# Kernel optimization log

Measured on AMD Instinct MI355X. Metric: run time of the kernel, lower is better.

The kernel has to match this reference:

```python
import math
import jax, jax.numpy as jnp
import numpy as np

# ---- MnnCoreModule constants (mnn_config defaults) ----
L = 0.05          # conductance
SL = math.sqrt(L)
VT = 20.0         # vol_th
VR = 0.0          # vol_rest
TREF = 5.0        # t_ref
CUT = 10.0        # cut_off
SQRT_PI_HALF = 0.8862269254527580


def _gl01(n):
    x, w = np.polynomial.legendre.leggauss(n)
    return (jnp.asarray((x + 1.0) / 2.0, jnp.float32),
            jnp.asarray(w / 2.0, jnp.float32))

A48, WA48 = _gl01(48)   # 1D quadrature nodes for G(x), E(x)
A32, WA32 = _gl01(32)   # outer nodes for H(x)
B32, WB32 = _gl01(32)   # inner nodes for H_pos
Q32, WQ32 = _gl01(32)   # nodes for semi-infinite inner integral (H_neg)
R32 = -jnp.log1p(-Q32)  # r = -log(1-q) maps (0,1) -> (0,inf)


def g_fn(x):
    """func_dawson: g(x) = sqrt(pi)/2 * exp(x^2) * (1 + erf(x)).
    Uses the asymptotic erfcx expansion for x << 0 (numerically stable)."""
    d = jnp.where(x >= -3.0, x, 0.0)
    direct = SQRT_PI_HALF * jnp.exp(d * d) * (1.0 + jax.scipy.special.erf(d))
    z = jnp.where(x < -3.0, -x, 3.0)
    z2 = z * z
    asym = (0.5 / z) * (1.0 - 0.5 / z2 + 0.75 / (z2 * z2) - 1.875 / (z2 * z2 * z2))
    return jnp.where(x >= -3.0, direct, asym)


def G_fn(x):
    """dawson1: G(x) = int_0^x g(t) dt (48-pt Gauss-Legendre, scaled)."""
    t = x[..., None] * A48
    return x * jnp.sum(WA48 * g_fn(t), axis=-1)


def E_fn(x):
    """int_0^x exp(t^2) dt for x >= 0."""
    t = x[..., None] * A48
    return x * jnp.sum(WA48 * jnp.exp(t * t), axis=-1)

# C0 = int_{-inf}^0 exp(-s^2) g(s)^2 ds (constant, high-accuracy quadrature)
_Q64, _WQ64 = _gl01(64)
_R64 = -jnp.log1p(-_Q64)
C0 = jnp.sum(_WQ64 * jnp.exp(-_R64 * _R64) * g_fn(-_R64) ** 2 / (1.0 - _Q64))


def _h_neg(t):
    """h(t) = exp(t^2) int_{-inf}^t exp(-s^2) g(s)^2 ds for t <= 0,
    via s = t - r, r = -log(1-q):  h(t) = int exp(2tr - r^2) g(t-r)^2 dr."""
    tt = t[..., None]
    integ = jnp.exp(2.0 * tt * R32 - R32 * R32) * g_fn(tt - R32) ** 2 / (1.0 - Q32)
    return jnp.sum(WQ32 * integ, axis=-1)


def H_neg(x):
    """double Dawson integral H(x) = int_0^x h(t) dt for x <= 0."""
    def step(aw):
        ai, wi = aw
        return wi * _h_neg(x * ai)
    terms = jax.lax.map(jax.checkpoint(step), (A32, WA32))  # [Ka, ...]
    return x * jnp.sum(terms, axis=0)


def H_pos(x):
    """H(x) for x >= 0: H = C0*E(x) + iint_{0<=s<=t<=x} e^{t^2-s^2} g(s)^2."""
    def step(aw):
        ai, wi = aw
        t = x * ai
        s = t[..., None] * B32
        inner = jnp.sum(WB32 * jnp.exp(-s * s) * g_fn(s) ** 2, axis=-1)
        return wi * ai * jnp.exp(t * t) * inner
    terms = jax.lax.map(jax.checkpoint(step), (A32, WA32))
    return C0 * E_fn(x) + x * x * jnp.sum(terms, axis=0)


def H_fn(x):
    return jnp.where(x >= 0.0, H_pos(jnp.maximum(x, 0.0)), H_neg(jnp.minimum(x, 0.0)))


def setup_inputs() -> dict:
    key = jax.random.key(0)
    k1, k2 = jax.random.split(key)
    u = 0.5 + jax.random.uniform(k1, (128, 1024), dtype=jnp.float32)  # [0.5, 1.5)
    raw = jax.random.uniform(k2, (128, 1024), dtype=jnp.float32) * 2.9
    s = jnp.where(raw < 0.4, 0.0, raw)
    return {"u": u, "s": s}


def reference(u, s):
    # region masks (mirrors _region0_idx)
    reg1 = (s > 0.0) & ((VT * L - u) < CUT * SL * s)
    reg0 = ~(s > 0.0)
    reg2 = reg0 & (u > VT * L)

    s_safe = jnp.where(reg1, s, 1.0)
    ub = jnp.where(reg1, (VT * L - u) / (SL * s_safe), 1.0)
    lb = jnp.where(reg1, (VR * L - u) / (SL * s_safe), 0.0)  # always <= 0

    # mean firing rate u_a
    dG = G_fn(ub) - G_fn(lb)
    u_a1 = 1.0 / ((2.0 / L) * dG + TREF)
    u2 = jnp.where(reg2, u, 2.0)
    logt = TREF - (1.0 / L) * jnp.log(1.0 - 1.0 / u2)
    u_a = jnp.where(reg1, u_a1, jnp.where(reg2, 1.0 / logt, 0.0))

    # std s_a via Fano factor
    dH = H_fn(ub) - H_neg(jnp.minimum(lb, 0.0))
    fano = jnp.where(reg1, (8.0 / (L * L)) * dH * u_a * u_a,
                     jnp.where(reg0, (u < 1.0).astype(u.dtype), 0.0))
    val = fano * u_a
    s_a = jnp.where(val > 0.0, jnp.sqrt(jnp.where(val > 0.0, val, 1.0)), 0.0)

    # linear response chi
    dg = g_fn(ub) - g_fn(lb)
    sa_safe = jnp.where(reg1 & (s_a > 0.0), s_a, 1.0)
    chi1 = u_a * u_a / sa_safe * dg * (2.0 / L ** 1.5)
    chi2 = math.sqrt(2.0 / L) / jnp.sqrt(logt) / jnp.sqrt(2.0 * u2 - 1.0)
    chi = jnp.where(reg1, chi1, jnp.where(reg2, chi2, 0.0))
    return (u_a, s_a, chi)
```

## Files before the change

kernel.cpp:

```cpp
#include <hip/hip_runtime.h>
#include <math.h>

#define SLf   0.22360679774997896f

#define NTAB   2048
#define XMIN   -17.0
#define XMAX   6.0
#define XMINf  -17.0f
#define DXf    (23.0f / 2047.0f)
#define INVDXf (2047.0f / 23.0f)

__device__ double dd_A48[48], dd_W48[48];
__device__ double dd_A32[32], dd_W32[32];
__device__ double dd_R32[32], dd_WQE32[32];
__device__ float f_A48[48], f_W48[48];
__device__ float f_A32[32], f_W32[32];
__device__ float f_R32[32], f_WQE32[32];
__device__ float f_C0;

__device__ float  htabf[NTAB];
__device__ float  innertabf[NTAB];
__device__ float4 tab4[NTAB];

__device__ double g_dbl(double x) {
    if (x >= -3.0) return 0.8862269254527580 * exp(x * x) * (1.0 + erf(x));
    double z = -x, iz2 = 1.0 / (z * z);
    return (0.5 / z) * (1.0 + iz2 * (-0.5 + iz2 * (0.75 - 1.875 * iz2)));
}

__device__ __forceinline__ float g_f32(float x) {
    if (x >= -3.0f) {
        return 0.88622692545275801f * __expf(x * x) * erfcf(-x);
    }
    float z = -x, iz = 1.0f / z, iz2 = iz * iz;
    return 0.5f * iz * (1.0f + iz2 * (-0.5f + iz2 * (0.75f - 1.875f * iz2)));
}

template <int N>
__device__ void gl_node_t(int i, const double* __restrict__ inv, double* x01, double* w01) {
    double z = cos(3.14159265358979323846 * ((double)i + 0.75) / ((double)N + 0.5));
    double pl = z, pm = 1.0, pp = 1.0;
    for (int it = 0; it < 6; ++it) {
        pm = 1.0; pl = z;
        #pragma unroll
        for (int k = 2; k <= N; ++k) {
            double pk = ((2.0 * k - 1.0) * z * pl - (k - 1.0) * pm) * inv[k];
            pm = pl; pl = pk;
        }
        pp = (double)N * (z * pl - pm) / (z * z - 1.0);
        z -= pl / pp;
    }
    pm = 1.0; pl = z;
    #pragma unroll
    for (int k = 2; k <= N; ++k) {
        double pk = ((2.0 * k - 1.0) * z * pl - (k - 1.0) * pm) * inv[k];
        pm = pl; pl = pk;
    }
    pp = (double)N * (z * pl - pm) / (z * z - 1.0);
    *x01 = 0.5 * (z + 1.0);
    *w01 = 1.0 / ((1.0 - z * z) * pp * pp);
}

__global__ void init_nodes() {
    __shared__ double s_inv[65];
    int i = threadIdx.x;
    if (i >= 2 && i <= 64) s_inv[i] = 1.0 / (double)i;
    __syncthreads();

    if (i < 48) {
        double x, w; gl_node_t<48>(i, s_inv, &x, &w);
        dd_A48[i] = x; dd_W48[i] = w;
        f_A48[i] = (float)x; f_W48[i] = (float)w;
    } else if (i >= 64 && i < 96) {
        int j = i - 64;
        double x, w; gl_node_t<32>(j, s_inv, &x, &w);
        dd_A32[j] = x; dd_W32[j] = w;
        f_A32[j] = (float)x; f_W32[j] = (float)w;
        f_R32[j] = (float)(-log1p(-x));
        f_WQE32[j] = (float)(w / (1.0 - x));
    } else if (i >= 128 && i < 192) {
        int j = i - 128;
        double x, w; gl_node_t<64>(j, s_inv, &x, &w);
        double r = -log1p(-x);
        double gv = g_dbl(-r);
        double term = w * exp(-r * r) * gv * gv / (1.0 - x);
        for (int off = 32; off > 0; off >>= 1)
            term += __shfl_down(term, off);
        if (j == 0) f_C0 = (float)term;
    }
}

__global__ __launch_bounds__(256) void init_tabs() {
    int gid = blockIdx.x * blockDim.x + threadIdx.x;
    int k = gid >> 2, p = gid & 3;
    if (k >= NTAB) return;
    float x = XMINf + DXf * (float)k;

    float aG = 0.0f;
    for (int q = 12 * p; q < 12 * p + 12; ++q)
        aG = fmaf(f_W48[q], g_f32(x * f_A48[q]), aG);

    float ah = 0.0f;
    for (int j = 8 * p; j < 8 * p + 8; ++j) {
        float r = f_R32[j];
        float gg = g_f32(x - r);
        ah = fmaf(f_WQE32[j], __expf((2.0f * x - r) * r) * gg * gg, ah);
    }

    float ai = 0.0f;
    for (int j = 8 * p; j < 8 * p + 8; ++j) {
        float s = x * f_A32[j];
        float gs = g_f32(s);
        ai = fmaf(f_W32[j], __expf(-s * s) * gs * gs, ai);
    }

    aG += __shfl_xor(aG, 1, 4); aG += __shfl_xor(aG, 2, 4);
    ah += __shfl_xor(ah, 1, 4); ah += __shfl_xor(ah, 2, 4);
    ai += __shfl_xor(ai, 1, 4); ai += __shfl_xor(ai, 2, 4);

    if (p == 0) {
        htabf[k] = ah;
        innertabf[k] = ai;
        float4 t; t.x = g_f32(x); t.y = x * aG; t.z = 0.0f; t.w = 0.0f;
        tab4[k] = t;
    }
}

__device__ __forceinline__ float interp1(const float* __restrict__ tab, float x) {
    float u = (x - XMINf) * INVDXf;
    u = fminf(fmaxf(u, 1.0f), (float)(NTAB - 3));
    int k = (int)u;
    if (k > NTAB - 3) k = NTAB - 3;
    float f = u - (float)k;
    float p0 = tab[k - 1], p1 = tab[k], p2 = tab[k + 1], p3 = tab[k + 2];
    return p1 + 0.5f * f * (p2 - p0 + f * (2.0f * p0 - 5.0f * p1 + 4.0f * p2 - p3
                 + f * (3.0f * (p1 - p2) + p3 - p0)));
}

__global__ __launch_bounds__(256) void init_H() {
    int gid = blockIdx.x * blockDim.x + threadIdx.x;
    int k = gid >> 2, p = gid & 3;
    if (k >= NTAB) return;
    float x = XMINf + DXf * (float)k;

    float H;
    if (x < 0.0f) {
        float acc = 0.0f;
        for (int i = 8 * p; i < 8 * p + 8; ++i)
            acc = fmaf(f_W32[i], interp1(htabf, x * f_A32[i]), acc);
        acc += __shfl_xor(acc, 1, 4); acc += __shfl_xor(acc, 2, 4);
        H = x * acc;
    } else {
        float aE = 0.0f;
        for (int q = 12 * p; q < 12 * p + 12; ++q) {
            float t = x * f_A48[q];
            aE = fmaf(f_W48[q], __expf(t * t), aE);
        }
        float aS = 0.0f;
        for (int i = 8 * p; i < 8 * p + 8; ++i) {
            float t = x * f_A32[i];
            aS = fmaf(f_W32[i] * f_A32[i], __expf(t * t) * interp1(innertabf, t), aS);
        }
        aE += __shfl_xor(aE, 1, 4); aE += __shfl_xor(aE, 2, 4);
        aS += __shfl_xor(aS, 1, 4); aS += __shfl_xor(aS, 2, 4);
        H = f_C0 * (x * aE) + x * x * aS;
    }
    if (p == 0) tab4[k].z = H;
}

__device__ __forceinline__ void cr_weights(float x, int* kk, float* w) {
    float u = (x - XMINf) * INVDXf;
    u = fminf(fmaxf(u, 1.0f), (float)(NTAB - 3));
    int k = (int)u;
    if (k > NTAB - 3) k = NTAB - 3;
    float f = u - (float)k;
    float f2 = f * f, f3 = f2 * f;
    w[0] = 0.5f * (-f + 2.0f * f2 - f3);
    w[1] = 1.0f + 0.5f * (-5.0f * f2 + 3.0f * f3);
    w[2] = 0.5f * (f + 4.0f * f2 - 3.0f * f3);
    w[3] = 0.5f * (f3 - f2);
    *kk = k;
}

__global__ __launch_bounds__(256) void mnn_main(const float* __restrict__ U,
        const float* __restrict__ S, float* __restrict__ out, int n) {
    int idx = blockIdx.x * blockDim.x + threadIdx.x;
    if (idx >= n) return;
    float u = U[idx], s = S[idx];
    float ua = 0.0f, sa = 0.0f, chi = 0.0f;

    bool sgt0 = (s > 0.0f);
    bool reg1 = sgt0 && ((1.0f - u) < 10.0f * SLf * s);

    if (reg1) {
        float inv = 1.0f / (SLf * s);
        float ub = (1.0f - u) * inv;
        float lb = -u * inv;

        int ku, kl; float wu[4], wl[4];
        cr_weights(ub, &ku, wu);
        cr_weights(lb, &kl, wl);
        float4 a0 = tab4[ku - 1], a1 = tab4[ku], a2 = tab4[ku + 1], a3 = tab4[ku + 2];
        float4 b0 = tab4[kl - 1], b1 = tab4[kl], b2 = tab4[kl + 1], b3 = tab4[kl + 2];

        float g_ub = wu[0]*a0.x + wu[1]*a1.x + wu[2]*a2.x + wu[3]*a3.x;
        float G_ub = wu[0]*a0.y + wu[1]*a1.y + wu[2]*a2.y + wu[3]*a3.y;
        float H_ub = wu[0]*a0.z + wu[1]*a1.z + wu[2]*a2.z + wu[3]*a3.z;
        float g_lb = wl[0]*b0.x + wl[1]*b1.x + wl[2]*b2.x + wl[3]*b3.x;
        float G_lb = wl[0]*b0.y + wl[1]*b1.y + wl[2]*b2.y + wl[3]*b3.y;
        float H_lb = wl[0]*b0.z + wl[1]*b1.z + wl[2]*b2.z + wl[3]*b3.z;

        float dG = G_ub - G_lb;
        float ua1 = 1.0f / (40.0f * dG + 5.0f);
        float dH = H_ub - H_lb;

        float fano = 3200.0f * dH * ua1 * ua1;
        float val = fano * ua1;
        float s_a = (val > 0.0f) ? sqrtf(val) : 0.0f;

        float dg = g_ub - g_lb;
        float sa_safe = (s_a > 0.0f) ? s_a : 1.0f;
        chi = ua1 * ua1 * dg * 178.88543819998318f / sa_safe;
        ua = ua1; sa = s_a;
    } else if (!sgt0 && u > 1.0f) {
        float logt = 5.0f - 20.0f * logf(1.0f - 1.0f / u);
        ua = 1.0f / logt;
        chi = 6.324555320336759f / (sqrtf(logt) * sqrtf(2.0f * u - 1.0f));
    }

    out[idx] = ua;
    out[n + idx] = sa;
    out[2 * n + idx] = chi;
}

extern "C" void kernel_launch(void* const* d_in, const int* in_sizes, int n_in,
                              void* d_out, int out_size, void* d_ws, size_t ws_size,
                              hipStream_t stream) {
    const float* u = (const float*)d_in[0];
    const float* s = (const float*)d_in[1];
    float* out = (float*)d_out;
    int n = in_sizes[0];

    init_nodes<<<dim3(1), dim3(256), 0, stream>>>();
    init_tabs<<<dim3((NTAB * 4 + 255) / 256), dim3(256), 0, stream>>>();
    init_H<<<dim3((NTAB * 4 + 255) / 256), dim3(256), 0, stream>>>();
    mnn_main<<<dim3((n + 255) / 256), dim3(256), 0, stream>>>(u, s, out, n);
}
```

Baseline: 30.51 us.

## Fuse three table-building kernels into one with per-block node generation

Replaces the init_nodes, init_tabs and init_H kernels with one build_tables kernel. Every block recomputes the Gauss-Legendre nodes into shared memory, and each 32-lane group builds one table entry. H is now computed by direct nested quadrature (32x32 g evaluations per entry) instead of interpolating from intermediate h/inner tables. This removes two kernel launches and their serialization, but adds redundant node computation in every block and much more arithmetic per table entry. Newton iterations for the nodes also drop from 6 to 4.

After: 29.13 us. 4.5% less time.

```diff
diff --git a/kernel.cpp b/kernel.cpp
--- a/kernel.cpp
+++ b/kernel.cpp
@@ -4,22 +4,10 @@
 #define SLf   0.22360679774997896f
 
 #define NTAB   2048
-#define XMIN   -17.0
-#define XMAX   6.0
 #define XMINf  -17.0f
 #define DXf    (23.0f / 2047.0f)
 #define INVDXf (2047.0f / 23.0f)
 
-__device__ double dd_A48[48], dd_W48[48];
-__device__ double dd_A32[32], dd_W32[32];
-__device__ double dd_R32[32], dd_WQE32[32];
-__device__ float f_A48[48], f_W48[48];
-__device__ float f_A32[32], f_W32[32];
-__device__ float f_R32[32], f_WQE32[32];
-__device__ float f_C0;
-
-__device__ float  htabf[NTAB];
-__device__ float  innertabf[NTAB];
 __device__ float4 tab4[NTAB];
 
 __device__ double g_dbl(double x) {
@@ -39,8 +27,8 @@
 template <int N>
 __device__ void gl_node_t(int i, const double* __restrict__ inv, double* x01, double* w01) {
     double z = cos(3.14159265358979323846 * ((double)i + 0.75) / ((double)N + 0.5));
-    double pl = z, pm = 1.0, pp = 1.0;
-    for (int it = 0; it < 6; ++it) {
+    double pl, pm, pp;
+    for (int it = 0; it < 4; ++it) {
         pm = 1.0; pl = z;
         #pragma unroll
         for (int k = 2; k <= N; ++k) {
@@ -61,111 +49,82 @@
     *w01 = 1.0 / ((1.0 - z * z) * pp * pp);
 }
 
-__global__ void init_nodes() {
+__global__ __launch_bounds__(256) void build_tables() {
     __shared__ double s_inv[65];
-    int i = threadIdx.x;
-    if (i >= 2 && i <= 64) s_inv[i] = 1.0 / (double)i;
+    __shared__ float sA48[48], sW48[48];
+    __shared__ float sA32[32], sW32[32], sR32[32], sWQ[32];
+    __shared__ float sC0;
+    int tid = threadIdx.x;
+    if (tid >= 2 && tid <= 64) s_inv[tid] = 1.0 / (double)tid;
     __syncthreads();
 
-    if (i < 48) {
-        double x, w; gl_node_t<48>(i, s_inv, &x, &w);
-        dd_A48[i] = x; dd_W48[i] = w;
-        f_A48[i] = (float)x; f_W48[i] = (float)w;
-    } else if (i >= 64 && i < 96) {
-        int j = i - 64;
+    if (tid < 48) {
+        double x, w; gl_node_t<48>(tid, s_inv, &x, &w);
+        sA48[tid] = (float)x; sW48[tid] = (float)w;
+    } else if (tid >= 64 && tid < 96) {
+        int j = tid - 64;
         double x, w; gl_node_t<32>(j, s_inv, &x, &w);
-        dd_A32[j] = x; dd_W32[j] = w;
-        f_A32[j] = (float)x; f_W32[j] = (float)w;
-        f_R32[j] = (float)(-log1p(-x));
-        f_WQE32[j] = (float)(w / (1.0 - x));
-    } else if (i >= 128 && i < 192) {
-        int j = i - 128;
+        sA32[j] = (float)x; sW32[j] = (float)w;
+        sR32[j] = (float)(-log1p(-x));
+        sWQ[j]  = (float)(w / (1.0 - x));
+    } else if (tid >= 128 && tid < 192) {
+        int j = tid - 128;
         double x, w; gl_node_t<64>(j, s_inv, &x, &w);
         double r = -log1p(-x);
         double gv = g_dbl(-r);
         double term = w * exp(-r * r) * gv * gv / (1.0 - x);
         for (int off = 32; off > 0; off >>= 1)
             term += __shfl_down(term, off);
-        if (j == 0) f_C0 = (float)term;
-    }
-}
-
-__global__ __launch_bounds__(256) void init_tabs() {
-    int gid = blockIdx.x * blockDim.x + threadIdx.x;
-    int k = gid >> 2, p = gid & 3;
-    if (k >= NTAB) return;
+        if (j == 0) sC0 = (float)term;
+    }
+    __syncthreads();
+
+    int k = blockIdx.x * 8 + (tid >> 5);
+    int i = tid & 31;
     float x = XMINf + DXf * (float)k;
 
-    float aG = 0.0f;
-    for (int q = 12 * p; q < 12 * p + 12; ++q)
-        aG = fmaf(f_W48[q], g_f32(x * f_A48[q]), aG);
-
-    float ah = 0.0f;
-    for (int j = 8 * p; j < 8 * p + 8; ++j) {
-        float r = f_R32[j];
-        float gg = g_f32(x - r);
-        ah = fmaf(f_WQE32[j], __expf((2.0f * x - r) * r) * gg * gg, ah);
-    }
-
-    float ai = 0.0f;
-    for (int j = 8 * p; j < 8 * p + 8; ++j) {
-        float s = x * f_A32[j];
-        float gs = g_f32(s);
-        ai = fmaf(f_W32[j], __expf(-s * s) * gs * gs, ai);
-    }
-
-    aG += __shfl_xor(aG, 1, 4); aG += __shfl_xor(aG, 2, 4);
-    ah += __shfl_xor(ah, 1, 4); ah += __shfl_xor(ah, 2, 4);
-    ai += __shfl_xor(ai, 1, 4); ai += __shfl_xor(ai, 2, 4);
-
-    if (p == 0) {
-        htabf[k] = ah;
-        innertabf[k] = ai;
-        float4 t; t.x = g_f32(x); t.y = x * aG; t.z = 0.0f; t.w = 0.0f;
-        tab4[k] = t;
-    }
-}
-
-__device__ __forceinline__ float interp1(const float* __restrict__ tab, float x) {
-    float u = (x - XMINf) * INVDXf;
-    u = fminf(fmaxf(u, 1.0f), (float)(NTAB - 3));
-    int k = (int)u;
-    if (k > NTAB - 3) k = NTAB - 3;
-    float f = u - (float)k;
-    float p0 = tab[k - 1], p1 = tab[k], p2 = tab[k + 1], p3 = tab[k + 2];
-    return p1 + 0.5f * f * (p2 - p0 + f * (2.0f * p0 - 5.0f * p1 + 4.0f * p2 - p3
-                 + f * (3.0f * (p1 - p2) + p3 - p0)));
-}
-
-__global__ __launch_bounds__(256) void init_H() {
-    int gid = blockIdx.x * blockDim.x + threadIdx.x;
-    int k = gid >> 2, p = gid & 3;
-    if (k >= NTAB) return;
-    float x = XMINf + DXf * (float)k;
-
-    float H;
+    float aG = sW48[i] * g_f32(x * sA48[i]);
+    if (i < 16) aG = fmaf(sW48[i + 32], g_f32(x * sA48[i + 32]), aG);
+
+    float Hp, aE = 0.0f;
+    float t = x * sA32[i];
     if (x < 0.0f) {
-        float acc = 0.0f;
-        for (int i = 8 * p; i < 8 * p + 8; ++i)
-            acc = fmaf(f_W32[i], interp1(htabf, x * f_A32[i]), acc);
-        acc += __shfl_xor(acc, 1, 4); acc += __shfl_xor(acc, 2, 4);
-        H = x * acc;
+        float h = 0.0f;
+        for (int j = 0; j < 32; ++j) {
+            float r = sR32[j];
+            float gg = g_f32(t - r);
+            h = fmaf(sWQ[j], __expf((2.0f * t - r) * r) * gg * gg, h);
+        }
+        Hp = sW32[i] * h;
     } else {
-        float aE = 0.0f;
-        for (int q = 12 * p; q < 12 * p + 12; ++q) {
-            float t = x * f_A48[q];
-            aE = fmaf(f_W48[q], __expf(t * t), aE);
-        }
-        float aS = 0.0f;
-        for (int i = 8 * p; i < 8 * p + 8; ++i) {
-            float t = x * f_A32[i];
-            aS = fmaf(f_W32[i] * f_A32[i], __expf(t * t) * interp1(innertabf, t), aS);
-        }
-        aE += __shfl_xor(aE, 1, 4); aE += __shfl_xor(aE, 2, 4);
-        aS += __shfl_xor(aS, 1, 4); aS += __shfl_xor(aS, 2, 4);
-        H = f_C0 * (x * aE) + x * x * aS;
-    }
-    if (p == 0) tab4[k].z = H;
+        float inner = 0.0f;
+        for (int j = 0; j < 32; ++j) {
+            float s = t * sA32[j];
+            float gs = g_f32(s);
+            inner = fmaf(sW32[j], __expf(-s * s) * gs * gs, inner);
+        }
+        Hp = sW32[i] * sA32[i] * __expf(t * t) * inner;
+        float t0 = x * sA48[i];
+        aE = sW48[i] * __expf(t0 * t0);
+        if (i < 16) {
+            float t1 = x * sA48[i + 32];
+            aE = fmaf(sW48[i + 32], __expf(t1 * t1), aE);
+        }
+    }
+
+    #pragma unroll
+    for (int off = 16; off > 0; off >>= 1) {
+        aG += __shfl_xor(aG, off, 32);
+        Hp += __shfl_xor(Hp, off, 32);
+        aE += __shfl_xor(aE, off, 32);
+    }
+
+    if (i == 0) {
+        float Hv = (x < 0.0f) ? x * Hp
+                              : sC0 * (x * aE) + x * x * Hp;
+        float4 e; e.x = g_f32(x); e.y = x * aG; e.z = Hv; e.w = 0.0f;
+        tab4[k] = e;
+    }
 }
 
 __device__ __forceinline__ void cr_weights(float x, int* kk, float* w) {
@@ -241,8 +200,6 @@
     float* out = (float*)d_out;
     int n = in_sizes[0];
 
-    init_nodes<<<dim3(1), dim3(256), 0, stream>>>();
-    init_tabs<<<dim3((NTAB * 4 + 255) / 256), dim3(256), 0, stream>>>();
-    init_H<<<dim3((NTAB * 4 + 255) / 256), dim3(256), 0, stream>>>();
+    build_tables<<<dim3(NTAB / 8), dim3(256), 0, stream>>>();
     mnn_main<<<dim3((n + 255) / 256), dim3(256), 0, stream>>>(u, s, out, n);
 }
```
